# Optimization experiments

Hardware: AMD Instinct MI355X
Metric: run time of the kernel (lower is better)

Reference implementation:

```python
import jax, jax.numpy as jnp
import numpy as np

BETA = 0.9
T = 16
THR = 1.0
SLOPE = 25.0  # snntorch surrogate.fast_sigmoid default slope


@jax.custom_vjp
def spike(x):
    # Heaviside forward, fast-sigmoid surrogate backward (snntorch fast_sigmoid)
    return (x > 0.0).astype(x.dtype)

def _spike_fwd(x):
    return spike(x), x

def _spike_bwd(x, g):
    return (g / (SLOPE * jnp.abs(x) + 1.0) ** 2,)

spike.defvjp(_spike_fwd, _spike_bwd)


def conv1d(x, w, b, pad):
    # x: (B, C_in, L), w: (C_out, C_in, K)
    y = jax.lax.conv_general_dilated(
        x, w, window_strides=(1,), padding=[(pad, pad)],
        dimension_numbers=("NCH", "OIH", "NCH"))
    return y + b[None, :, None]


def lif(cur, mem):
    # snntorch Leaky, reset_mechanism='subtract', threshold=1.0.
    # reset spike is computed from the PREVIOUS membrane and detached.
    reset = jax.lax.stop_gradient((mem > THR).astype(cur.dtype))
    mem = BETA * mem + cur - reset * THR
    spk = spike(mem - THR)
    return spk, mem


def setup_inputs() -> dict:
    key = jax.random.key(0)
    ks = jax.random.split(key, 14)

    def u(k, shape, fan_in):
        bound = 1.0 / np.sqrt(fan_in)
        return jax.random.uniform(k, shape, jnp.float32, -bound, bound)

    x = jax.random.normal(ks[0], (2048, 2, 128), dtype=jnp.float32)
    W1 = u(ks[1], (256, 2, 5), 2 * 5);    b1 = u(ks[2], (256,), 2 * 5)
    W2 = u(ks[3], (128, 256, 3), 256 * 3); b2 = u(ks[4], (128,), 256 * 3)
    W3 = u(ks[5], (64, 128, 3), 128 * 3);  b3 = u(ks[6], (64,), 128 * 3)
    W4 = u(ks[7], (2, 64, 3), 64 * 3);     b4 = u(ks[8], (2,), 64 * 3)
    fw1 = u(ks[9], (100, 256), 256);       fb1 = u(ks[10], (100,), 256)
    fw2 = u(ks[11], (40, 100), 100);       fb2 = u(ks[12], (40,), 100)
    return {"x": x, "W1": W1, "b1": b1, "W2": W2, "b2": b2,
            "W3": W3, "b3": b3, "W4": W4, "b4": b4,
            "fw1": fw1, "fb1": fb1, "fw2": fw2, "fb2": fb2}


def reference(x, W1, b1, W2, b2, W3, b3, W4, b4, fw1, fb1, fw2, fb2):
    B, _, L = x.shape
    f32 = x.dtype
    # conv1 input is constant across timesteps -> hoist (same math)
    cur1 = conv1d(x, W1, b1, 2)
    init = (jnp.zeros((B, 256, L), f32), jnp.zeros((B, 128, L), f32),
            jnp.zeros((B, 64, L), f32), jnp.zeros((B, 2, L), f32),
            jnp.zeros((B, 100), f32), jnp.zeros((B, 40), f32))

    def step(carry, _):
        m1, m2, m3, m4, m5, acc = carry
        s1, m1 = lif(cur1, m1)
        s2, m2 = lif(conv1d(s1, W2, b2, 1), m2)
        s3, m3 = lif(conv1d(s2, W3, b3, 1), m3)
        s4, m4 = lif(conv1d(s3, W4, b4, 1), m4)
        flat = s4.reshape(B, -1)                      # (B, 256)
        s5, m5 = lif(flat @ fw1.T + fb1, m5)
        acc = acc + s5 @ fw2.T + fb2
        return (m1, m2, m3, m4, m5, acc), None

    (_, _, _, _, _, acc), _ = jax.lax.scan(step, init, None, length=T)
    return acc / T
```

## Files before the change

### kernel.cpp

```cpp
#include <hip/hip_runtime.h>
#include <stdint.h>

#define BETA 0.9f

typedef unsigned short u16;
typedef unsigned char u8;
typedef _Float16 f16x8 __attribute__((ext_vector_type(8)));
typedef float f32x4 __attribute__((ext_vector_type(4)));

__device__ __forceinline__ void async_copy16(const void* g, void* l) {
  __builtin_amdgcn_global_load_lds(
      (const __attribute__((address_space(1))) uint32_t*)g,
      (__attribute__((address_space(3))) uint32_t*)l, 16, 0, 0);
}

__device__ __forceinline__ f16x8 expandB(uint32_t byte) {
  union { uint32_t u[4]; f16x8 v; } r;
  uint32_t z = byte | (byte << 15);
#pragma unroll
  for (int m = 0; m < 4; ++m)
    r.u[m] = ((z >> (2 * m)) & 0x10001u) << 12;
  return r.v;
}

__global__ void prep_kernel(const float* __restrict__ W2, const float* __restrict__ W3,
                            const float* __restrict__ fw1, const float* __restrict__ fw2,
                            u16* __restrict__ A2c, u16* __restrict__ A3c,
                            float* __restrict__ fw1T, float* __restrict__ fw2T) {
  int o = blockIdx.x * 256 + threadIdx.x;
  if (o < 98304) {
    int tap = o >> 15, r = o & 32767, co = r >> 8, ci = r & 255;
    float w = W2[(co * 256 + ci) * 3 + tap];
    float h = (float)(_Float16)w;
    _Float16 hv = (_Float16)(h * 2048.0f);
    _Float16 mv = (_Float16)((w - h) * 2048.0f);
    u16 hb, mb;
    __builtin_memcpy(&hb, &hv, 2);
    __builtin_memcpy(&mb, &mv, 2);
    int c = ci >> 5, cl = ci & 31;
    int g = ((cl >> 3) ^ ((co >> 1) & 3)) & 3;
    int pos = g * 8 + (cl & 7);
    A2c[(((c * 2 + 0) * 3 + tap) * 128 + co) * 32 + pos] = hb;
    A2c[(((c * 2 + 1) * 3 + tap) * 128 + co) * 32 + pos] = mb;
  }
  int o2 = o - 98304;
  if (o2 >= 0 && o2 < 24576) {
    int tap = o2 >> 13, r = o2 & 8191, co = r >> 7, ci = r & 127;
    float w = W3[(co * 128 + ci) * 3 + tap];
    float h = (float)(_Float16)w;
    _Float16 hv = (_Float16)(h * 2048.0f);
    _Float16 mv = (_Float16)((w - h) * 2048.0f);
    u16 hb, mb;
    __builtin_memcpy(&hb, &hv, 2);
    __builtin_memcpy(&mb, &mv, 2);
    int c = ci >> 5, cl = ci & 31;
    int g = ((cl >> 3) ^ ((co >> 1) & 3)) & 3;
    int pos = g * 8 + (cl & 7);
    A3c[(((c * 2 + 0) * 3 + tap) * 64 + co) * 32 + pos] = hb;
    A3c[(((c * 2 + 1) * 3 + tap) * 64 + co) * 32 + pos] = mb;
  }
  int o3 = o - (98304 + 24576);
  if (o3 >= 0 && o3 < 25600) {
    int f = o3 / 100, i = o3 % 100;
    fw1T[o3] = fw1[i * 256 + f];
  }
  int o4 = o - (98304 + 24576 + 25600);
  if (o4 >= 0 && o4 < 4000) {
    int i = o4 / 40, j = o4 % 40;
    fw2T[o4] = fw2[j * 100 + i];
  }
}

__global__ __launch_bounds__(256) void conv1_lif_kernel(
    const float* __restrict__ x, const float* __restrict__ W1,
    const float* __restrict__ b1, u8* __restrict__ SBT2) {
  __shared__ float xl[2][132];
  __shared__ u16 bl[8][128];
  int b = blockIdx.x, g = blockIdx.y;
  int tid = threadIdx.x;
  for (int i = tid; i < 264; i += 256) {
    int ci = i / 132, idx = i % 132, lg = idx - 2;
    xl[ci][idx] = (lg >= 0 && lg < 128) ? x[(b * 2 + ci) * 128 + lg] : 0.0f;
  }
  __syncthreads();
  int cosub = tid >> 5, tx = tid & 31;
  int co = g * 8 + cosub;
  float w[2][5];
#pragma unroll
  for (int ci = 0; ci < 2; ++ci)
#pragma unroll
    for (int k = 0; k < 5; ++k) w[ci][k] = W1[(co * 2 + ci) * 5 + k];
  float bias = b1[co];
  float cur[4];
#pragma unroll
  for (int j = 0; j < 4; ++j) {
    float acc = bias;
#pragma unroll
    for (int ci = 0; ci < 2; ++ci)
#pragma unroll
      for (int k = 0; k < 5; ++k) acc += w[ci][k] * xl[ci][4 * tx + j + k];
    cur[j] = acc;
  }
  float m[4] = {0.f, 0.f, 0.f, 0.f}, sp[4] = {0.f, 0.f, 0.f, 0.f};
  uint32_t bits[4] = {0u, 0u, 0u, 0u};
#pragma unroll
  for (int t = 0; t < 16; ++t) {
#pragma unroll
    for (int j = 0; j < 4; ++j) {
      m[j] = BETA * m[j] + cur[j] - sp[j];
      bool s = m[j] > 1.0f;
      bits[j] |= ((uint32_t)s) << t;
      sp[j] = s ? 1.0f : 0.0f;
    }
  }
#pragma unroll
  for (int j = 0; j < 4; ++j) bl[cosub][4 * tx + j] = (u16)bits[j];
  __syncthreads();
  if (tid < 128) {
    int l = tid;
    uint32_t wv[8];
#pragma unroll
    for (int j = 0; j < 8; ++j) wv[j] = bl[j][l];
    uint32_t ov[4];
#pragma unroll
    for (int k = 0; k < 4; ++k) {
      uint32_t v = 0;
#pragma unroll
      for (int tt = 0; tt < 4; ++tt) {
        int t = k * 4 + tt;
        uint32_t by = 0;
#pragma unroll
        for (int j = 0; j < 8; ++j) by |= ((wv[j] >> t) & 1u) << j;
        v |= by << (8 * tt);
      }
      ov[k] = v;
    }
    *(uint4*)(SBT2 + ((size_t)(b * 128 + l) * 32 + g) * 16) =
        make_uint4(ov[0], ov[1], ov[2], ov[3]);
  }
}

template <int CIN, int COUT, bool SBTOUT>
__global__ __launch_bounds__(256, 3) void conv_mfma_kernel(
    const u8* __restrict__ SBT, const u16* __restrict__ Agc,
    const float* __restrict__ bias, void* __restrict__ outp) {
  constexpr int NPHYS = CIN / 32;
  constexpr int NVIRT = 2 * NPHYS;
  constexpr int MT = COUT / 32;
  constexpr int GB = CIN / 8;
  constexpr int ABYTES = 3 * COUT * 32 * 2;
  constexpr int AW = ABYTES / 4;
  constexpr int AISS = AW / 1024;
  constexpr int EPB = 19456 + COUT * 8 * 2;
  constexpr int LDSSZ = (2 * ABYTES > EPB) ? 2 * ABYTES : EPB;
  __shared__ __align__(16) char lds[LDSSZ];

  int b = blockIdx.x, lb = blockIdx.y * 8;
  int tid = threadIdx.x, lane = tid & 63, wid = tid >> 6;
  int wx = wid & 1, wy = wid >> 1;
  int q = lane >> 4, xx = lane & 15;
  int mbase = wy * (COUT / 2);
  int lw = lb + wx * 4;
  int qs8 = (q ^ ((xx >> 1) & 3)) * 8;

  f32x4 acc[MT][4];
#pragma unroll
  for (int mt = 0; mt < MT; ++mt)
#pragma unroll
    for (int nt = 0; nt < 4; ++nt) acc[mt][nt] = (f32x4){0.f, 0.f, 0.f, 0.f};

  uint32_t byt[6];
#pragma unroll
  for (int u = 0; u < 6; ++u) {
    int l_in = lw + u - 1;
    byt[u] = ((unsigned)l_in < 128u)
                 ? (uint32_t)SBT[((size_t)(b * 128 + l_in) * GB + q) * 16 + xx]
                 : 0u;
  }
  {
    const char* gsrc = (const char*)Agc + (size_t)wid * AW + lane * 16;
    char* ldst = lds + wid * AW;
#pragma unroll
    for (int i = 0; i < AISS; ++i) async_copy16(gsrc + i * 1024, ldst + i * 1024);
  }

  f16x8 Bf[6];
#pragma unroll 2
  for (int v = 0; v < NVIRT; ++v) {
    __syncthreads();
    if (v + 1 < NVIRT) {
      const char* gsrc = (const char*)Agc + (size_t)(v + 1) * ABYTES +
                         (size_t)wid * AW + lane * 16;
      char* ldst = lds + ((v + 1) & 1) * ABYTES + wid * AW;
#pragma unroll
      for (int i = 0; i < AISS; ++i) async_copy16(gsrc + i * 1024, ldst + i * 1024);
    }
    if ((v & 1) == 0) {
#pragma unroll
      for (int u = 0; u < 6; ++u) Bf[u] = expandB(byt[u]);
      int pn = (v >> 1) + 1;
      if (pn < NPHYS) {
#pragma unroll
        for (int u = 0; u < 6; ++u) {
          int l_in = lw + u - 1;
          byt[u] = ((unsigned)l_in < 128u)
                       ? (uint32_t)SBT[((size_t)(b * 128 + l_in) * GB + pn * 4 + q) * 16 + xx]
                       : 0u;
        }
      }
    }
    const u16* Asv = (const u16*)(lds + (v & 1) * ABYTES);
#pragma unroll
    for (int tap = 0; tap < 3; ++tap)
#pragma unroll
      for (int mt = 0; mt < MT; ++mt) {
        f16x8 Af = *(const f16x8*)(Asv + ((size_t)(tap * COUT + mbase + mt * 16 + xx)) * 32 + qs8);
#pragma unroll
        for (int nt = 0; nt < 4; ++nt)
          acc[mt][nt] = __builtin_amdgcn_mfma_f32_16x16x32_f16(
              Af, Bf[nt + tap], acc[mt][nt], 0, 0, 0);
      }
  }
  __syncthreads();

  float* scr = (float*)(void*)lds + wid * 1216;
  u16* bl = (u16*)(lds + 19456);
#pragma unroll
  for (int mt = 0; mt < MT; ++mt) {
#pragma unroll
    for (int nt = 0; nt < 4; ++nt)
#pragma unroll
      for (int r = 0; r < 4; ++r)
        scr[(nt * 16 + q * 4 + r) * 19 + xx] = acc[mt][nt][r];
    __syncthreads();
    int co = mbase + mt * 16 + xx;
    float bc = bias[co];
    const float* rowp = scr + (q * 16 + xx) * 19;
    float mm = 0.f, sp = 0.f;
    uint32_t bits = 0;
#pragma unroll
    for (int t = 0; t < 16; ++t) {
      float cur = rowp[t] + bc;
      mm = BETA * mm + cur - sp;
      bool s = mm > 1.0f;
      bits |= ((uint32_t)s) << t;
      sp = s ? 1.0f : 0.0f;
    }
    bl[co * 8 + wx * 4 + q] = (u16)bits;
    __syncthreads();
  }

  if constexpr (SBTOUT) {
    constexpr int GBo = COUT / 8;
    if (tid < GBo * 8) {
      int g = tid & (GBo - 1), ll = tid / GBo;
      uint32_t wv[8];
#pragma unroll
      for (int j = 0; j < 8; ++j) wv[j] = bl[(8 * g + j) * 8 + ll];
      uint32_t ov[4];
#pragma unroll
      for (int k = 0; k < 4; ++k) {
        uint32_t v = 0;
#pragma unroll
        for (int tt = 0; tt < 4; ++tt) {
          int t = k * 4 + tt;
          uint32_t by = 0;
#pragma unroll
          for (int j = 0; j < 8; ++j) by |= ((wv[j] >> t) & 1u) << j;
          v |= by << (8 * tt);
        }
        ov[k] = v;
      }
      *(uint4*)((u8*)outp + ((size_t)(b * 128 + lb + ll) * GBo + g) * 16) =
          make_uint4(ov[0], ov[1], ov[2], ov[3]);
    }
  } else {
    if (tid < COUT) {
      uint4 v = *(const uint4*)(bl + tid * 8);
      *(uint4*)((u16*)outp + ((size_t)b * COUT + tid) * 128 + lb) = v;
    }
  }
}

__global__ __launch_bounds__(256) void head_kernel(
    const u16* __restrict__ s3bits, const float* __restrict__ W4,
    const float* __restrict__ b4, const float* __restrict__ fw1T,
    const float* __restrict__ fb1, const float* __restrict__ fw2T,
    const float* __restrict__ fb2, float* __restrict__ out) {
  __shared__ u16 s3l[64][130];
  __shared__ float W4l[384];
  __shared__ u16 flat4[256];
  __shared__ u16 s5b[100];
  int b = blockIdx.x, tid = threadIdx.x;

  for (int i = tid; i < 64 * 130; i += 256) {
    int ci = i / 130, idx = i % 130, lg = idx - 1;
    s3l[ci][idx] = (lg >= 0 && lg < 128) ? s3bits[((size_t)b * 64 + ci) * 128 + lg] : (u16)0;
  }
  for (int i = tid; i < 384; i += 256) W4l[i] = W4[i];
  __syncthreads();

  {
    int co = tid >> 7, l = tid & 127;
    float acc4[16];
#pragma unroll
    for (int t = 0; t < 16; ++t) acc4[t] = 0.f;
    for (int ci = 0; ci < 64; ++ci) {
#pragma unroll
      for (int k = 0; k < 3; ++k) {
        float wv = W4l[(co * 64 + ci) * 3 + k];
        uint32_t msk = s3l[ci][l + k];
#pragma unroll
        for (int t = 0; t < 16; ++t)
          acc4[t] = fmaf(wv, (float)((msk >> t) & 1u), acc4[t]);
      }
    }
    float bc = b4[co];
    float m = 0.f, sp = 0.f;
    uint32_t bits = 0;
#pragma unroll
    for (int t = 0; t < 16; ++t) {
      m = BETA * m + (acc4[t] + bc) - sp;
      bool s = m > 1.0f;
      bits |= ((uint32_t)s) << t;
      sp = s ? 1.0f : 0.0f;
    }
    flat4[tid] = (u16)bits;
  }
  __syncthreads();

  if (tid < 100) {
    float acc5[16];
#pragma unroll
    for (int t = 0; t < 16; ++t) acc5[t] = 0.f;
    for (int f = 0; f < 256; ++f) {
      float wv = fw1T[f * 100 + tid];
      uint32_t msk = flat4[f];
#pragma unroll
      for (int t = 0; t < 16; ++t)
        acc5[t] = fmaf(wv, (float)((msk >> t) & 1u), acc5[t]);
    }
    float bc = fb1[tid];
    float m = 0.f, sp = 0.f;
    uint32_t bits = 0;
#pragma unroll
    for (int t = 0; t < 16; ++t) {
      m = BETA * m + (acc5[t] + bc) - sp;
      bool s = m > 1.0f;
      bits |= ((uint32_t)s) << t;
      sp = s ? 1.0f : 0.0f;
    }
    s5b[tid] = (u16)bits;
  }
  __syncthreads();

  if (tid < 40) {
    float a = 0.f;
    for (int i = 0; i < 100; ++i) {
      float wv = fw2T[i * 40 + tid];
      a = fmaf(wv, (float)__popc((uint32_t)s5b[i]), a);
    }
    out[b * 40 + tid] = a * 0.0625f + fb2[tid];
  }
}

extern "C" void kernel_launch(void* const* d_in, const int* in_sizes, int n_in,
                              void* d_out, int out_size, void* d_ws, size_t ws_size,
                              hipStream_t stream) {
  const float* x   = (const float*)d_in[0];
  const float* W1  = (const float*)d_in[1];
  const float* b1  = (const float*)d_in[2];
  const float* W2  = (const float*)d_in[3];
  const float* b2  = (const float*)d_in[4];
  const float* W3  = (const float*)d_in[5];
  const float* b3  = (const float*)d_in[6];
  const float* W4  = (const float*)d_in[7];
  const float* b4  = (const float*)d_in[8];
  const float* fw1 = (const float*)d_in[9];
  const float* fb1 = (const float*)d_in[10];
  const float* fw2 = (const float*)d_in[11];
  const float* fb2 = (const float*)d_in[12];
  float* out = (float*)d_out;

  char* ws = (char*)d_ws;
  u16*   A2c  = (u16*)(ws);
  u16*   A3c  = (u16*)(ws + 393216);
  float* fw1T = (float*)(ws + 491520);
  float* fw2T = (float*)(ws + 593920);
  u8*    SBT2 = (u8*)(ws + 610304);
  u8*    SBT3 = (u8*)(ws + 610304 + 134217728);
  u16*   s3b  = (u16*)(ws + 610304 + 134217728 + 67108864);

  prep_kernel<<<dim3(596), dim3(256), 0, stream>>>(W2, W3, fw1, fw2, A2c, A3c, fw1T, fw2T);
  conv1_lif_kernel<<<dim3(2048, 32), dim3(256), 0, stream>>>(x, W1, b1, SBT2);
  conv_mfma_kernel<256, 128, true><<<dim3(2048, 16), dim3(256), 0, stream>>>(SBT2, A2c, b2, SBT3);
  conv_mfma_kernel<128, 64, false><<<dim3(2048, 16), dim3(256), 0, stream>>>(SBT3, A3c, b3, s3b);
  head_kernel<<<dim3(2048), dim3(256), 0, stream>>>(s3b, W4, b4, fw1T, fb1, fw2T, fb2, out);
}
```

Before: 2.068 ms.

## Split conv2 output channels across grid z to shrink per-block LDS and registers

The MFMA conv kernel now handles 64 output channels per block, with a third grid dimension selecting the channel tile. The prep kernel re-lays out the W2 weights so each channel tile is contiguous. This cuts accumulator registers and the LDS double buffer so launch bounds can target 6 blocks per CU for more latency hiding. The cost is that conv2 reads and expands its spike input twice, once per channel tile, and launches twice as many blocks.

```diff
diff --git a/kernel.cpp b/kernel.cpp
--- a/kernel.cpp
+++ b/kernel.cpp
@@ -38,10 +38,11 @@
     __builtin_memcpy(&hb, &hv, 2);
     __builtin_memcpy(&mb, &mv, 2);
     int c = ci >> 5, cl = ci & 31;
+    int ct = co >> 6, col = co & 63;
     int g = ((cl >> 3) ^ ((co >> 1) & 3)) & 3;
     int pos = g * 8 + (cl & 7);
-    A2c[(((c * 2 + 0) * 3 + tap) * 128 + co) * 32 + pos] = hb;
-    A2c[(((c * 2 + 1) * 3 + tap) * 128 + co) * 32 + pos] = mb;
+    A2c[((((c * 2 + 0) * 2 + ct) * 3 + tap) * 64 + col) * 32 + pos] = hb;
+    A2c[((((c * 2 + 1) * 2 + ct) * 3 + tap) * 64 + col) * 32 + pos] = mb;
   }
   int o2 = o - 98304;
   if (o2 >= 0 && o2 < 24576) {
@@ -141,25 +142,24 @@
 }
 
 template <int CIN, int COUT, bool SBTOUT>
-__global__ __launch_bounds__(256, 3) void conv_mfma_kernel(
+__global__ __launch_bounds__(256, 6) void conv_mfma_kernel(
     const u8* __restrict__ SBT, const u16* __restrict__ Agc,
     const float* __restrict__ bias, void* __restrict__ outp) {
   constexpr int NPHYS = CIN / 32;
   constexpr int NVIRT = 2 * NPHYS;
-  constexpr int MT = COUT / 32;
+  constexpr int NCT = COUT / 64;
+  constexpr int MT = 2;
   constexpr int GB = CIN / 8;
-  constexpr int ABYTES = 3 * COUT * 32 * 2;
+  constexpr int ABYTES = 3 * 64 * 32 * 2;
   constexpr int AW = ABYTES / 4;
   constexpr int AISS = AW / 1024;
-  constexpr int EPB = 19456 + COUT * 8 * 2;
-  constexpr int LDSSZ = (2 * ABYTES > EPB) ? 2 * ABYTES : EPB;
-  __shared__ __align__(16) char lds[LDSSZ];
-
-  int b = blockIdx.x, lb = blockIdx.y * 8;
+  __shared__ __align__(16) char lds[2 * ABYTES];
+
+  int b = blockIdx.x, lb = blockIdx.y * 8, ct = blockIdx.z;
   int tid = threadIdx.x, lane = tid & 63, wid = tid >> 6;
   int wx = wid & 1, wy = wid >> 1;
   int q = lane >> 4, xx = lane & 15;
-  int mbase = wy * (COUT / 2);
+  int mloc = wy * 32;
   int lw = lb + wx * 4;
   int qs8 = (q ^ ((xx >> 1) & 3)) * 8;
 
@@ -178,7 +178,8 @@
                  : 0u;
   }
   {
-    const char* gsrc = (const char*)Agc + (size_t)wid * AW + lane * 16;
+    const char* gsrc = (const char*)Agc + (size_t)ct * ABYTES +
+                       (size_t)wid * AW + lane * 16;
     char* ldst = lds + wid * AW;
 #pragma unroll
     for (int i = 0; i < AISS; ++i) async_copy16(gsrc + i * 1024, ldst + i * 1024);
@@ -189,7 +190,7 @@
   for (int v = 0; v < NVIRT; ++v) {
     __syncthreads();
     if (v + 1 < NVIRT) {
-      const char* gsrc = (const char*)Agc + (size_t)(v + 1) * ABYTES +
+      const char* gsrc = (const char*)Agc + ((size_t)(v + 1) * NCT + ct) * ABYTES +
                          (size_t)wid * AW + lane * 16;
       char* ldst = lds + ((v + 1) & 1) * ABYTES + wid * AW;
 #pragma unroll
@@ -214,7 +215,7 @@
     for (int tap = 0; tap < 3; ++tap)
 #pragma unroll
       for (int mt = 0; mt < MT; ++mt) {
-        f16x8 Af = *(const f16x8*)(Asv + ((size_t)(tap * COUT + mbase + mt * 16 + xx)) * 32 + qs8);
+        f16x8 Af = *(const f16x8*)(Asv + ((size_t)(tap * 64 + mloc + mt * 16 + xx)) * 32 + qs8);
 #pragma unroll
         for (int nt = 0; nt < 4; ++nt)
           acc[mt][nt] = __builtin_amdgcn_mfma_f32_16x16x32_f16(
@@ -233,8 +234,8 @@
       for (int r = 0; r < 4; ++r)
         scr[(nt * 16 + q * 4 + r) * 19 + xx] = acc[mt][nt][r];
     __syncthreads();
-    int co = mbase + mt * 16 + xx;
-    float bc = bias[co];
+    int col = mloc + mt * 16 + xx;
+    float bc = bias[ct * 64 + col];
     const float* rowp = scr + (q * 16 + xx) * 19;
     float mm = 0.f, sp = 0.f;
     uint32_t bits = 0;
@@ -246,14 +247,14 @@
       bits |= ((uint32_t)s) << t;
       sp = s ? 1.0f : 0.0f;
     }
-    bl[co * 8 + wx * 4 + q] = (u16)bits;
+    bl[col * 8 + wx * 4 + q] = (u16)bits;
     __syncthreads();
   }
 
   if constexpr (SBTOUT) {
     constexpr int GBo = COUT / 8;
-    if (tid < GBo * 8) {
-      int g = tid & (GBo - 1), ll = tid / GBo;
+    if (tid < 64) {
+      int g = tid & 7, ll = tid >> 3;
       uint32_t wv[8];
 #pragma unroll
       for (int j = 0; j < 8; ++j) wv[j] = bl[(8 * g + j) * 8 + ll];
@@ -271,13 +272,13 @@
         }
         ov[k] = v;
       }
-      *(uint4*)((u8*)outp + ((size_t)(b * 128 + lb + ll) * GBo + g) * 16) =
+      *(uint4*)((u8*)outp + ((size_t)(b * 128 + lb + ll) * GBo + ct * 8 + g) * 16) =
           make_uint4(ov[0], ov[1], ov[2], ov[3]);
     }
   } else {
-    if (tid < COUT) {
+    if (tid < 64) {
       uint4 v = *(const uint4*)(bl + tid * 8);
-      *(uint4*)((u16*)outp + ((size_t)b * COUT + tid) * 128 + lb) = v;
+      *(uint4*)((u16*)outp + ((size_t)b * COUT + ct * 64 + tid) * 128 + lb) = v;
     }
   }
 }
@@ -393,7 +394,7 @@
 
   prep_kernel<<<dim3(596), dim3(256), 0, stream>>>(W2, W3, fw1, fw2, A2c, A3c, fw1T, fw2T);
   conv1_lif_kernel<<<dim3(2048, 32), dim3(256), 0, stream>>>(x, W1, b1, SBT2);
-  conv_mfma_kernel<256, 128, true><<<dim3(2048, 16), dim3(256), 0, stream>>>(SBT2, A2c, b2, SBT3);
-  conv_mfma_kernel<128, 64, false><<<dim3(2048, 16), dim3(256), 0, stream>>>(SBT3, A3c, b3, s3b);
+  conv_mfma_kernel<256, 128, true><<<dim3(2048, 16, 2), dim3(256), 0, stream>>>(SBT2, A2c, b2, SBT3);
+  conv_mfma_kernel<128, 64, false><<<dim3(2048, 16, 1), dim3(256), 0, stream>>>(SBT3, A3c, b3, s3b);
   head_kernel<<<dim3(2048), dim3(256), 0, stream>>>(s3b, W4, b4, fw1T, fb1, fw2T, fb2, out);
 }
```

After: 2.569 ms. +24.2%, slower.
